# Kernel tuning notes

Measured on AMD Instinct MI355X. Metric: run time of the kernel, lower is better.

Reference implementation:

```python
import jax, jax.numpy as jnp
import numpy as np
import math

NO, NR, E = 100000, 1000, 1000000
DO, DR, DE, H, OM = 64, 32, 4, 64, 32


def setup_inputs() -> dict:
    key = jax.random.key(0)
    ks = jax.random.split(key, 20)
    s = lambda k, sh: jax.random.normal(k, sh, dtype=jnp.float32) * 0.05
    inp = {
        'x_order': jax.random.normal(ks[0], (NO, DO), dtype=jnp.float32),
        'x_rider': jax.random.normal(ks[1], (NR, DR), dtype=jnp.float32),
        'edge_attr': jax.random.normal(ks[2], (E, DE), dtype=jnp.float32),
        'order_idx': jax.random.randint(ks[3], (E,), 0, NO),
        'rider_idx': jax.random.randint(ks[4], (E,), 0, NR),
        'omega_encoded': jax.random.normal(ks[5], (OM,), dtype=jnp.float32),
        # TransformerConv params (heads=1)
        'Wk': s(ks[6], (DO, H)), 'bk': jnp.zeros((H,), jnp.float32),
        'Wq': s(ks[7], (DR, H)), 'bq': jnp.zeros((H,), jnp.float32),
        'Wv': s(ks[8], (DO, H)), 'bv': jnp.zeros((H,), jnp.float32),
        'We': s(ks[9], (DE, H)),  # lin_edge, bias=False in PyG
        'Wskip': s(ks[10], (DR, H)), 'bskip': jnp.zeros((H,), jnp.float32),
        # order_proj
        'Wp': s(ks[11], (DO, H)), 'bp': jnp.zeros((H,), jnp.float32),
        # residual MLP: Linear(2H+OM,128) -> ReLU -> Linear(128,1)
        'W1': s(ks[12], (2 * H + OM, 128)), 'b1': jnp.zeros((128,), jnp.float32),
        'W2': s(ks[13], (128, 1)), 'b2': jnp.zeros((1,), jnp.float32),
    }
    return inp


def _segment_softmax(alpha, seg, num_segments):
    m = jax.ops.segment_max(alpha, seg, num_segments=num_segments)
    m = jnp.where(jnp.isfinite(m), m, 0.0)
    ex = jnp.exp(alpha - m[seg])
    denom = jax.ops.segment_sum(ex, seg, num_segments=num_segments)
    return ex / (denom[seg] + 1e-16)


def reference(x_order, x_rider, edge_attr, order_idx, rider_idx, omega_encoded,
              Wk, bk, Wq, bq, Wv, bv, We, Wskip, bskip, Wp, bp, W1, b1, W2, b2):
    scale = 1.0 / math.sqrt(H)
    # TransformerConv((order, rider) -> rider), heads=1, edge_dim
    q = x_rider @ Wq + bq            # [NR, H]
    k = x_order @ Wk + bk            # [NO, H]
    v = x_order @ Wv + bv            # [NO, H]
    e = edge_attr @ We               # [E, H]
    k_j = k[order_idx] + e           # [E, H]
    v_j = v[order_idx] + e           # [E, H]
    alpha = jnp.sum(q[rider_idx] * k_j, axis=-1) * scale  # [E]
    alpha = _segment_softmax(alpha, rider_idx, NR)
    agg = jax.ops.segment_sum(alpha[:, None] * v_j, rider_idx, num_segments=NR)  # [NR, H]
    rider_emb = agg + x_rider @ Wskip + bskip  # root/skip connection

    # edge scoring
    order_proj = x_order @ Wp + bp   # [NO, H]
    oe = order_proj[order_idx]       # [E, H]
    re = rider_emb[rider_idx]        # [E, H]
    dot = jnp.sum(oe * re, axis=-1) * scale  # [E]
    omega_expand = jnp.broadcast_to(omega_encoded[None, :], (oe.shape[0], OM))
    resid_in = jnp.concatenate([oe, re, omega_expand], axis=-1)  # [E, 2H+OM]
    hmid = jax.nn.relu(resid_in @ W1 + b1)
    resid = (hmid @ W2 + b2)[:, 0]
    return jnp.clip(dot + resid, -10.0, 10.0)
```

## Files before the change

### kernel.cpp

```cpp
#include <hip/hip_runtime.h>
#include <hip/hip_bf16.h>
#include <math.h>
#include <stdint.h>

#define NO_N 100000
#define NR_N 1000
#define E_N  1000000
#define SB     500
#define SCHUNK 2000
#define KVP_TILES 1563
#define KVP_BLKS 1024
#define MAXTILES 17008

typedef short bf16x8 __attribute__((ext_vector_type(8)));
typedef float floatx4 __attribute__((ext_vector_type(4)));

__device__ __forceinline__ unsigned short bfu(float x) {
    union { __hip_bfloat16 h; unsigned short u; } c;
    c.h = __float2bfloat16(x);
    return c.u;
}
__device__ __forceinline__ float bflo(unsigned int u) {
    return __uint_as_float(u << 16);
}
__device__ __forceinline__ float bfhi(unsigned int u) {
    return __uint_as_float(u & 0xffff0000u);
}

__global__ __launch_bounds__(256) void k_front(
    const float* __restrict__ xr,
    const float* __restrict__ Wq, const float* __restrict__ bq,
    const float* __restrict__ Wskip, const float* __restrict__ bskip,
    const float* __restrict__ We,
    float* __restrict__ q, float* __restrict__ skip, float* __restrict__ t,
    const float* __restrict__ W1, const float* __restrict__ b1,
    const float* __restrict__ omega, float* __restrict__ b1eff,
    unsigned short* __restrict__ w1t,
    const float* __restrict__ x,
    const float* __restrict__ Wk, const float* __restrict__ bk,
    const float* __restrict__ Wv, const float* __restrict__ bv,
    const float* __restrict__ Wp, const float* __restrict__ bp,
    unsigned short* __restrict__ kb, unsigned short* __restrict__ vb,
    unsigned short* __restrict__ pb,
    const int* __restrict__ ridx, int* __restrict__ ghist)
{
    __shared__ __align__(16) char smem[9216];
    const int tid = threadIdx.x;
    const int b = blockIdx.x;

    if (b < 250) {
        float* sx = (float*)smem;
        float* sq = sx + 128;
        int rbase = b * 4;
        if (tid < 128) {
            int rl = tid >> 5, d = tid & 31;
            sx[rl * 32 + d] = xr[(rbase + rl) * 32 + d];
        }
        __syncthreads();
        int rl = tid >> 6, h = tid & 63;
        int r = rbase + rl;
        float aq = bq[h], as = bskip[h];
        #pragma unroll 4
        for (int d = 0; d < 32; ++d) {
            float xv = sx[rl * 32 + d];
            aq += xv * Wq[d * 64 + h];
            as += xv * Wskip[d * 64 + h];
        }
        sq[rl * 64 + h] = aq;
        q[r * 64 + h] = aq;
        skip[r * 64 + h] = as;
        __syncthreads();
        if (tid < 16) {
            int rl2 = tid >> 2, d = tid & 3;
            float acc = 0.f;
            for (int hh = 0; hh < 64; ++hh)
                acc += We[d * 64 + hh] * sq[rl2 * 64 + hh];
            t[(rbase + rl2) * 4 + d] = acc;
        }
    } else if (b == 250) {
        if (tid < 128) {
            float acc = b1[tid];
            #pragma unroll 4
            for (int j = 0; j < 32; ++j)
                acc += omega[j] * W1[(128 + j) * 128 + tid];
            b1eff[tid] = acc;
        }
        for (int idx = tid; idx < 64 * 128; idx += 256) {
            int n = idx >> 6, k = idx & 63;
            w1t[idx] = bfu(W1[k * 128 + n]);
        }
    } else if (b < 251 + KVP_BLKS) {
        unsigned short* sX = (unsigned short*)smem;
        const int wave = tid >> 6, lane = tid & 63;
        const int l15 = lane & 15, quad = lane >> 4;

        bf16x8 bfr[3][2];
        float bias[3];
        unsigned short* outT[3];
        int colc[3];
        #pragma unroll
        for (int ct = 0; ct < 3; ++ct) {
            int n = wave * 48 + ct * 16 + l15;
            int table = n >> 6, c = n & 63;
            const float* W  = (table == 0) ? Wk : (table == 1) ? Wv : Wp;
            const float* bb = (table == 0) ? bk : (table == 1) ? bv : bp;
            bias[ct] = bb[c];
            colc[ct] = c;
            outT[ct] = (table == 0) ? kb : (table == 1) ? vb : pb;
            #pragma unroll
            for (int kf = 0; kf < 2; ++kf) {
                bf16x8 f;
                #pragma unroll
                for (int j = 0; j < 8; ++j)
                    f[j] = (short)bfu(W[(size_t)(kf * 32 + quad * 8 + j) * 64 + c]);
                bfr[ct][kf] = f;
            }
        }

        const int srl = tid >> 2;
        const int sqt = (tid & 3) * 16;

        for (int tile = b - 251; tile < KVP_TILES; tile += KVP_BLKS) {
            int rowbase = tile * 64;
            {
                int row = rowbase + srl;
                unsigned short* dst = sX + srl * 72 + sqt;
                if (row < NO_N) {
                    const float4* src = (const float4*)(x + (size_t)row * 64 + sqt);
                    #pragma unroll
                    for (int i = 0; i < 4; ++i) {
                        float4 a = src[i];
                        ushort4 u = { bfu(a.x), bfu(a.y), bfu(a.z), bfu(a.w) };
                        *(ushort4*)(dst + i * 4) = u;
                    }
                } else {
                    ushort4 z = {0, 0, 0, 0};
                    #pragma unroll
                    for (int i = 0; i < 4; ++i) *(ushort4*)(dst + i * 4) = z;
                }
            }
            __syncthreads();

            floatx4 acc[4][3];
            #pragma unroll
            for (int rt = 0; rt < 4; ++rt)
                #pragma unroll
                for (int ct = 0; ct < 3; ++ct)
                    acc[rt][ct] = (floatx4){bias[ct], bias[ct], bias[ct], bias[ct]};

            #pragma unroll
            for (int rt = 0; rt < 4; ++rt) {
                const unsigned short* ar = sX + (size_t)(rt * 16 + l15) * 72 + quad * 8;
                bf16x8 a0 = *(const bf16x8*)(ar);
                bf16x8 a1 = *(const bf16x8*)(ar + 32);
                #pragma unroll
                for (int ct = 0; ct < 3; ++ct) {
                    floatx4 c = acc[rt][ct];
                    c = __builtin_amdgcn_mfma_f32_16x16x32_bf16(a0, bfr[ct][0], c, 0, 0, 0);
                    c = __builtin_amdgcn_mfma_f32_16x16x32_bf16(a1, bfr[ct][1], c, 0, 0, 0);
                    acc[rt][ct] = c;
                }
            }

            #pragma unroll
            for (int rt = 0; rt < 4; ++rt) {
                int rb = rowbase + rt * 16 + quad * 4;
                #pragma unroll
                for (int ct = 0; ct < 3; ++ct) {
                    unsigned short* o = outT[ct];
                    size_t cbase = colc[ct];
                    #pragma unroll
                    for (int g = 0; g < 4; ++g) {
                        int row = rb + g;
                        if (row < NO_N)
                            o[(size_t)row * 64 + cbase] = bfu(acc[rt][ct][g]);
                    }
                }
            }
            __syncthreads();
        }
    } else {
        int* hc = (int*)smem;
        int hb = b - (251 + KVP_BLKS);
        for (int i = tid; i < NR_N; i += 256) hc[i] = 0;
        __syncthreads();
        int s = hb * SCHUNK;
        for (int i = s + tid; i < s + SCHUNK; i += 256)
            atomicAdd(&hc[ridx[i]], 1);
        __syncthreads();
        for (int i = tid; i < NR_N; i += 256)
            ghist[i * SB + hb] = hc[i];
    }
}

__global__ __launch_bounds__(512) void k_colscan(const int* __restrict__ ghist,
                                                 int* __restrict__ gpre,
                                                 int* __restrict__ counts)
{
    __shared__ int s[512];
    int tid = threadIdx.x, r = blockIdx.x;
    int v = (tid < SB) ? ghist[r * SB + tid] : 0;
    s[tid] = v;
    __syncthreads();
    for (int off = 1; off < 512; off <<= 1) {
        int tv = (tid >= off) ? s[tid - off] : 0;
        __syncthreads();
        s[tid] += tv;
        __syncthreads();
    }
    if (tid < SB) gpre[r * SB + tid] = s[tid] - v;
    if (tid == 511) counts[r] = s[511];
}

__global__ __launch_bounds__(1024) void k_scan(const int* __restrict__ counts,
                                               int* __restrict__ offsets,
                                               int* __restrict__ tilestart)
{
    __shared__ int s[1024];
    int tid = threadIdx.x;
    int c = (tid < NR_N) ? counts[tid] : 0;
    s[tid] = c;
    __syncthreads();
    for (int off = 1; off < 1024; off <<= 1) {
        int tv = (tid >= off) ? s[tid - off] : 0;
        __syncthreads();
        s[tid] += tv;
        __syncthreads();
    }
    if (tid < NR_N) offsets[tid] = s[tid] - c;
    if (tid == NR_N - 1) offsets[NR_N] = s[tid];
    __syncthreads();
    int tc = (tid < NR_N) ? ((c + 63) >> 6) : 0;
    s[tid] = tc;
    __syncthreads();
    for (int off = 1; off < 1024; off <<= 1) {
        int tv = (tid >= off) ? s[tid - off] : 0;
        __syncthreads();
        s[tid] += tv;
        __syncthreads();
    }
    if (tid < NR_N) tilestart[tid] = s[tid] - tc;
    if (tid == NR_N - 1) tilestart[NR_N] = s[tid];
}

__global__ __launch_bounds__(256) void k_trec(const int* __restrict__ tilestart,
                                              const int* __restrict__ offsets,
                                              int4* __restrict__ trec)
{
    int nt = tilestart[NR_N];
    int t = blockIdx.x * 256 + threadIdx.x;
    if (t >= nt) return;
    int lo = 0, hi = NR_N - 1;
    while (lo < hi) {
        int mid = (lo + hi + 1) >> 1;
        if (tilestart[mid] <= t) lo = mid; else hi = mid - 1;
    }
    trec[t] = make_int4(lo, offsets[lo] + ((t - tilestart[lo]) << 6),
                        offsets[lo + 1], 0);
}

__global__ __launch_bounds__(1024) void k_scatter2(
    const int* __restrict__ ridx, const int* __restrict__ oidx,
    const float* __restrict__ ea, const float* __restrict__ t,
    const int* __restrict__ offsets, const int* __restrict__ gpre,
    const int* __restrict__ ghist,
    int4* __restrict__ spack, int* __restrict__ so, int* __restrict__ rank)
{
    __shared__ int stmp[1024];
    __shared__ int lpre[NR_N];
    __shared__ int lcur[NR_N];
    __shared__ int gbase[NR_N];
    __shared__ __align__(16) int4 sbuf[SCHUNK];
    __shared__ int spos[SCHUNK];

    const int tid = threadIdx.x, b = blockIdx.x;

    int v = (tid < NR_N) ? ghist[tid * SB + b] : 0;
    stmp[tid] = v;
    __syncthreads();
    for (int off = 1; off < 1024; off <<= 1) {
        int tv = (tid >= off) ? stmp[tid - off] : 0;
        __syncthreads();
        stmp[tid] += tv;
        __syncthreads();
    }
    if (tid < NR_N) {
        lpre[tid] = stmp[tid] - v;
        lcur[tid] = 0;
        gbase[tid] = offsets[tid] + gpre[tid * SB + b];
    }
    __syncthreads();

    int s = b * SCHUNK;
    for (int i = s + tid; i < s + SCHUNK; i += 1024) {
        int r = ridx[i];
        int o = oidx[i];
        float4 e4 = *(const float4*)(ea + (size_t)i * 4);
        float4 t4 = *(const float4*)(t + r * 4);
        float h = e4.x * t4.x + e4.y * t4.y + e4.z * t4.z + e4.w * t4.w;
        int old = atomicAdd(&lcur[r], 1);
        int lpos = lpre[r] + old;
        int gp = gbase[r] + old;
        int4 pk;
        pk.x = o;
        pk.y = __float_as_int(h);
        pk.z = (int)((unsigned)bfu(e4.x) | ((unsigned)bfu(e4.y) << 16));
        pk.w = (int)((unsigned)bfu(e4.z) | ((unsigned)bfu(e4.w) << 16));
        sbuf[lpos] = pk;
        spos[lpos] = gp;
        rank[i] = gp;
    }
    __syncthreads();

    for (int l = tid; l < SCHUNK; l += 1024) {
        int4 pk = sbuf[l];
        int gp = spos[l];
        spack[gp] = pk;
        so[gp] = pk.x;
    }
}

__global__ __launch_bounds__(512) void k_rider(
    const int* __restrict__ offsets, const int4* __restrict__ spack,
    const float* __restrict__ q,
    const unsigned short* __restrict__ kb, const unsigned short* __restrict__ vb,
    const float* __restrict__ We, const float* __restrict__ skip,
    const float* __restrict__ W1, const float* __restrict__ b1eff,
    unsigned short* __restrict__ embb, float* __restrict__ Br)
{
    __shared__ float sQ[64];
    __shared__ int2 sOX[8][64];
    __shared__ float rv[8][64];
    __shared__ float re4[8][4];
    __shared__ float rd[8];

    int r = blockIdx.x;
    int wave = threadIdx.x >> 6, lane = threadIdx.x & 63;
    if (threadIdx.x < 64) sQ[threadIdx.x] = q[r * 64 + threadIdx.x];
    __syncthreads();

    int beg = offsets[r], end = offsets[r + 1];
    int cnt = end - beg;
    int chunk = (cnt + 7) >> 3;
    int s0 = beg + wave * chunk;
    int s1 = min(s0 + chunk, end);

    float av0 = 0.f, av1 = 0.f, av2 = 0.f, av3 = 0.f;
    float dsum = 0.f;
    float ag0 = 0.f, ag1 = 0.f, ag2 = 0.f, ag3 = 0.f;
    const float2* sQ2 = (const float2*)sQ;

    for (int jb = s0; jb < s1; jb += 64) {
        int j = jb + lane;
        bool valid = (j < s1);
        int4 pk = make_int4(0, 0, 0, 0);
        if (valid) pk = spack[j];
        int oo = pk.x;
        float h = __int_as_float(pk.y);

        const uint4* krow = (const uint4*)(kb + (size_t)oo * 64);
        uint4 K0 = krow[0], K1 = krow[1], K2 = krow[2], K3 = krow[3];
        uint4 K4 = krow[4], K5 = krow[5], K6 = krow[6], K7 = krow[7];
        float a0 = h, a1 = 0.f, a2 = 0.f, a3 = 0.f;
        #define DOT8(Kv, base, A) { \
            float2 qa = sQ2[(base) + 0]; \
            A = fmaf(bflo(Kv.x), qa.x, A); A = fmaf(bfhi(Kv.x), qa.y, A); \
            float2 qb = sQ2[(base) + 1]; \
            A = fmaf(bflo(Kv.y), qb.x, A); A = fmaf(bfhi(Kv.y), qb.y, A); \
            float2 qc = sQ2[(base) + 2]; \
            A = fmaf(bflo(Kv.z), qc.x, A); A = fmaf(bfhi(Kv.z), qc.y, A); \
            float2 qd = sQ2[(base) + 3]; \
            A = fmaf(bflo(Kv.w), qd.x, A); A = fmaf(bfhi(Kv.w), qd.y, A); }
        DOT8(K0, 0, a0) DOT8(K1, 4, a1) DOT8(K2, 8, a2) DOT8(K3, 12, a3)
        DOT8(K4, 16, a0) DOT8(K5, 20, a1) DOT8(K6, 24, a2) DOT8(K7, 28, a3)
        #undef DOT8
        float acc = (a0 + a1) + (a2 + a3);

        float exv = valid ? __expf(acc * 0.125f) : 0.f;
        dsum += exv;
        unsigned int ez = (unsigned int)pk.z, ew = (unsigned int)pk.w;
        ag0 = fmaf(exv, bflo(ez), ag0);
        ag1 = fmaf(exv, bfhi(ez), ag1);
        ag2 = fmaf(exv, bflo(ew), ag2);
        ag3 = fmaf(exv, bfhi(ew), ag3);

        sOX[wave][lane] = make_int2(oo, __float_as_int(exv));

        int nn = min(s1 - jb, 64);
        int i = 0;
        for (; i + 8 <= nn; i += 8) {
            int2 x0 = sOX[wave][i + 0], x1 = sOX[wave][i + 1];
            int2 x2 = sOX[wave][i + 2], x3 = sOX[wave][i + 3];
            int2 x4 = sOX[wave][i + 4], x5 = sOX[wave][i + 5];
            int2 x6 = sOX[wave][i + 6], x7 = sOX[wave][i + 7];
            unsigned short u0 = vb[(size_t)x0.x * 64 + lane];
            unsigned short u1 = vb[(size_t)x1.x * 64 + lane];
            unsigned short u2 = vb[(size_t)x2.x * 64 + lane];
            unsigned short u3 = vb[(size_t)x3.x * 64 + lane];
            unsigned short u4 = vb[(size_t)x4.x * 64 + lane];
            unsigned short u5 = vb[(size_t)x5.x * 64 + lane];
            unsigned short u6 = vb[(size_t)x6.x * 64 + lane];
            unsigned short u7 = vb[(size_t)x7.x * 64 + lane];
            av0 = fmaf(__int_as_float(x0.y), __uint_as_float((unsigned int)u0 << 16), av0);
            av1 = fmaf(__int_as_float(x1.y), __uint_as_float((unsigned int)u1 << 16), av1);
            av2 = fmaf(__int_as_float(x2.y), __uint_as_float((unsigned int)u2 << 16), av2);
            av3 = fmaf(__int_as_float(x3.y), __uint_as_float((unsigned int)u3 << 16), av3);
            av0 = fmaf(__int_as_float(x4.y), __uint_as_float((unsigned int)u4 << 16), av0);
            av1 = fmaf(__int_as_float(x5.y), __uint_as_float((unsigned int)u5 << 16), av1);
            av2 = fmaf(__int_as_float(x6.y), __uint_as_float((unsigned int)u6 << 16), av2);
            av3 = fmaf(__int_as_float(x7.y), __uint_as_float((unsigned int)u7 << 16), av3);
        }
        for (; i < nn; ++i) {
            int2 xx = sOX[wave][i];
            unsigned short uu = vb[(size_t)xx.x * 64 + lane];
            av0 = fmaf(__int_as_float(xx.y), __uint_as_float((unsigned int)uu << 16), av0);
        }
    }

    float aggv = (av0 + av1) + (av2 + av3);

    #pragma unroll
    for (int m = 1; m < 64; m <<= 1) {
        dsum += __shfl_xor(dsum, m);
        ag0 += __shfl_xor(ag0, m);
        ag1 += __shfl_xor(ag1, m);
        ag2 += __shfl_xor(ag2, m);
        ag3 += __shfl_xor(ag3, m);
    }

    rv[wave][lane] = aggv;
    if (lane == 0) {
        rd[wave] = dsum;
        re4[wave][0] = ag0; re4[wave][1] = ag1;
        re4[wave][2] = ag2; re4[wave][3] = ag3;
    }
    __syncthreads();
    if (threadIdx.x < 64) {
        int l = threadIdx.x;
        float av = 0.f, ds = 0.f, a0 = 0.f, a1 = 0.f, a2 = 0.f, a3 = 0.f;
        #pragma unroll
        for (int w = 0; w < 8; ++w) {
            av += rv[w][l]; ds += rd[w];
            a0 += re4[w][0]; a1 += re4[w][1]; a2 += re4[w][2]; a3 += re4[w][3];
        }
        float corr = a0 * We[0 * 64 + l] + a1 * We[1 * 64 + l]
                   + a2 * We[2 * 64 + l] + a3 * We[3 * 64 + l];
        float val = (av + corr) / (ds + 1e-16f) + skip[r * 64 + l];
        embb[r * 64 + l] = bfu(val);
        sQ[l] = val;
    }
    __syncthreads();
    if (threadIdx.x < 128) {
        int c = threadIdx.x;
        float a = b1eff[c];
        #pragma unroll 8
        for (int d = 0; d < 64; ++d)
            a = fmaf(sQ[d], W1[(size_t)(64 + d) * 128 + c], a);
        Br[r * 128 + c] = a;
    }
}

__global__ __launch_bounds__(256) void k_edge2(
    const int* __restrict__ so, const int4* __restrict__ trec,
    const int* __restrict__ tilestart,
    const unsigned short* __restrict__ pb, const unsigned short* __restrict__ embb,
    const float* __restrict__ Br, const unsigned short* __restrict__ w1t,
    const float* __restrict__ W2, const float* __restrict__ b2,
    float* __restrict__ tmp)
{
    const int tid = threadIdx.x;
    const int wave = tid >> 6;
    const int lane = tid & 63;
    const int l15 = lane & 15;
    const int quad = lane >> 4;

    bf16x8 bfr[8][2];
    floatx4 w2q[8];
    #pragma unroll
    for (int ctl = 0; ctl < 8; ++ctl) {
        int n = ctl * 16 + l15;
        bfr[ctl][0] = *(const bf16x8*)(w1t + n * 64 + quad * 8);
        bfr[ctl][1] = *(const bf16x8*)(w1t + n * 64 + 32 + quad * 8);
        w2q[ctl] = *(const floatx4*)(W2 + ctl * 16 + quad * 4);
    }
    float b2v = b2[0];
    const int ntiles = tilestart[NR_N];
    const bf16x8 z8 = (bf16x8){0, 0, 0, 0, 0, 0, 0, 0};

    union U4B { uint4 u; bf16x8 b; };

    const int stride = gridDim.x * 4;
    int tile = blockIdx.x * 4 + wave;
    if (tile >= ntiles) return;

    int4 rr = trec[tile];
    int o_rt[4];
    #pragma unroll
    for (int rt = 0; rt < 4; ++rt)
        o_rt[rt] = so[min(rr.y + rt * 16 + l15, rr.z - 1)];

    for (; tile < ntiles; tile += stride) {
        const int r = rr.x, jb = rr.y, jend = rr.z;

        U4B A0[4], A1[4];
        #pragma unroll
        for (int rt = 0; rt < 4; ++rt) {
            const unsigned short* rowp = pb + (size_t)o_rt[rt] * 64 + quad * 8;
            A0[rt].u = *(const uint4*)(rowp);
            A1[rt].u = *(const uint4*)(rowp + 32);
        }

        int4 rrn = trec[min(tile + stride, ntiles - 1)];
        int o_nx[4];
        #pragma unroll
        for (int rt = 0; rt < 4; ++rt)
            o_nx[rt] = so[min(rrn.y + rt * 16 + l15, rrn.z - 1)];

        const unsigned short* eb = embb + r * 64;
        bf16x8 b80 = z8, b81 = z8;
        if (l15 == 0) {
            b80 = *(const bf16x8*)(eb + quad * 8);
            b81 = *(const bf16x8*)(eb + 32 + quad * 8);
        }

        const float* brrow = Br + r * 128;

        #pragma unroll
        for (int rt = 0; rt < 4; ++rt) {
            float s = 0.f;
            #pragma unroll
            for (int ctl = 0; ctl < 8; ++ctl) {
                floatx4 c = *(const floatx4*)(brrow + ctl * 16 + quad * 4);
                c = __builtin_amdgcn_mfma_f32_16x16x32_bf16(bfr[ctl][0], A0[rt].b, c, 0, 0, 0);
                c = __builtin_amdgcn_mfma_f32_16x16x32_bf16(bfr[ctl][1], A1[rt].b, c, 0, 0, 0);
                #pragma unroll
                for (int g = 0; g < 4; ++g)
                    s = fmaf(fmaxf(c[g], 0.f), w2q[ctl][g], s);
            }
            floatx4 c8 = (floatx4){0.f, 0.f, 0.f, 0.f};
            c8 = __builtin_amdgcn_mfma_f32_16x16x32_bf16(b80, A0[rt].b, c8, 0, 0, 0);
            c8 = __builtin_amdgcn_mfma_f32_16x16x32_bf16(b81, A1[rt].b, c8, 0, 0, 0);

            s += __shfl_xor(s, 16);
            s += __shfl_xor(s, 32);

            if (quad == 0) {
                int pos = jb + rt * 16 + l15;
                if (pos < jend) {
                    float v = s + 0.125f * c8[0] + b2v;
                    tmp[pos] = fminf(fmaxf(v, -10.f), 10.f);
                }
            }
        }

        rr = rrn;
        #pragma unroll
        for (int rt = 0; rt < 4; ++rt) o_rt[rt] = o_nx[rt];
    }
}

__global__ __launch_bounds__(256) void k_perm(const int* __restrict__ rank,
                                              const float* __restrict__ tmp,
                                              float* __restrict__ out)
{
    int i = blockIdx.x * 256 + threadIdx.x;
    if (i < E_N) out[i] = tmp[rank[i]];
}

extern "C" void kernel_launch(void* const* d_in, const int* in_sizes, int n_in,
                              void* d_out, int out_size, void* d_ws, size_t ws_size,
                              hipStream_t stream)
{
    const float* x_order   = (const float*)d_in[0];
    const float* x_rider   = (const float*)d_in[1];
    const float* edge_attr = (const float*)d_in[2];
    const int*   order_idx = (const int*)d_in[3];
    const int*   rider_idx = (const int*)d_in[4];
    const float* omega     = (const float*)d_in[5];
    const float* Wk = (const float*)d_in[6];  const float* bk = (const float*)d_in[7];
    const float* Wq = (const float*)d_in[8];  const float* bq = (const float*)d_in[9];
    const float* Wv = (const float*)d_in[10]; const float* bv = (const float*)d_in[11];
    const float* We = (const float*)d_in[12];
    const float* Wskip = (const float*)d_in[13]; const float* bskip = (const float*)d_in[14];
    const float* Wp = (const float*)d_in[15]; const float* bp = (const float*)d_in[16];
    const float* W1 = (const float*)d_in[17]; const float* b1 = (const float*)d_in[18];
    const float* W2 = (const float*)d_in[19]; const float* b2 = (const float*)d_in[20];
    float* out = (float*)d_out;

    unsigned short* ws_kb = (unsigned short*)d_ws;
    unsigned short* ws_vb = ws_kb + (size_t)NO_N * 64;
    unsigned short* ws_pb = ws_vb + (size_t)NO_N * 64;
    int4* ws_spack = (int4*)(ws_pb + (size_t)NO_N * 64);
    float* ws_tmp  = (float*)ws_spack;
    int*  ws_so    = (int*)(ws_spack + E_N);
    int*  ws_rank  = ws_so + E_N;
    float* wsf     = (float*)(ws_rank + E_N);
    float* ws_q    = wsf;
    float* ws_skip = ws_q + NR_N * 64;
    unsigned short* ws_embb = (unsigned short*)(ws_skip + NR_N * 64);
    float* ws_t    = (float*)(ws_embb + NR_N * 64);
    float* ws_b1e  = ws_t + NR_N * 4;
    unsigned short* ws_w1t = (unsigned short*)(ws_b1e + 128);
    float* ws_Br   = (float*)(ws_w1t + 128 * 64);
    int* ws_counts  = (int*)(ws_Br + NR_N * 128);
    int* ws_offsets = ws_counts + NR_N;
    int* ws_tilest  = ws_offsets + NR_N + 8;
    int* ws_ghist   = ws_tilest + NR_N + 8;
    int* ws_gpre    = ws_ghist + NR_N * SB;
    int4* ws_trec   = (int4*)(((uintptr_t)(ws_gpre + NR_N * SB) + 15) & ~(uintptr_t)15);

    k_front<<<251 + KVP_BLKS + SB, 256, 0, stream>>>(
        x_rider, Wq, bq, Wskip, bskip, We, ws_q, ws_skip, ws_t,
        W1, b1, omega, ws_b1e, ws_w1t,
        x_order, Wk, bk, Wv, bv, Wp, bp, ws_kb, ws_vb, ws_pb,
        rider_idx, ws_ghist);
    k_colscan<<<NR_N, 512, 0, stream>>>(ws_ghist, ws_gpre, ws_counts);
    k_scan<<<1, 1024, 0, stream>>>(ws_counts, ws_offsets, ws_tilest);
    k_trec<<<(MAXTILES + 255) / 256, 256, 0, stream>>>(ws_tilest, ws_offsets, ws_trec);
    k_scatter2<<<SB, 1024, 0, stream>>>(rider_idx, order_idx, edge_attr, ws_t,
                                        ws_offsets, ws_gpre, ws_ghist,
                                        ws_spack, ws_so, ws_rank);
    k_rider<<<NR_N, 512, 0, stream>>>(ws_offsets, ws_spack, ws_q,
                                      ws_kb, ws_vb, We, ws_skip,
                                      W1, ws_b1e, ws_embb, ws_Br);
    k_edge2<<<1024, 256, 0, stream>>>(ws_so, ws_trec, ws_tilest,
                                      ws_pb, ws_embb, ws_Br, ws_w1t, W2, b2, ws_tmp);
    k_perm<<<(E_N + 255) / 256, 256, 0, stream>>>(ws_rank, ws_tmp, out);
}
```

Measured before the change: 276.4 us.

## Fuse column scan with global scan via last-block pattern, merge trec into scatter

Result: slower. 508.4 us (+83.9%).

```diff
diff --git a/kernel.cpp b/kernel.cpp
--- a/kernel.cpp
+++ b/kernel.cpp
@@ -6,11 +6,12 @@
 #define NO_N 100000
 #define NR_N 1000
 #define E_N  1000000
-#define SB     500
-#define SCHUNK 2000
+#define SB     250
+#define SCHUNK 4000
 #define KVP_TILES 1563
 #define KVP_BLKS 1024
 #define MAXTILES 17008
+#define TREC_BLKS ((MAXTILES + 1023) / 1024)
 
 typedef short bf16x8 __attribute__((ext_vector_type(8)));
 typedef float floatx4 __attribute__((ext_vector_type(4)));
@@ -42,7 +43,8 @@
     const float* __restrict__ Wp, const float* __restrict__ bp,
     unsigned short* __restrict__ kb, unsigned short* __restrict__ vb,
     unsigned short* __restrict__ pb,
-    const int* __restrict__ ridx, int* __restrict__ ghist)
+    const int* __restrict__ ridx, int* __restrict__ ghist,
+    int* __restrict__ done)
 {
     __shared__ __align__(16) char smem[9216];
     const int tid = threadIdx.x;
@@ -78,6 +80,7 @@
             t[(rbase + rl2) * 4 + d] = acc;
         }
     } else if (b == 250) {
+        if (tid == 0) done[0] = 0;
         if (tid < 128) {
             float acc = b1[tid];
             #pragma unroll 4
@@ -193,31 +196,36 @@
     }
 }
 
-__global__ __launch_bounds__(512) void k_colscan(const int* __restrict__ ghist,
-                                                 int* __restrict__ gpre,
-                                                 int* __restrict__ counts)
+__global__ __launch_bounds__(1024) void k_mid(
+    const int* __restrict__ ghist, int* __restrict__ gpre,
+    int* __restrict__ counts, int* __restrict__ offsets,
+    int* __restrict__ tilestart, int* __restrict__ done)
 {
-    __shared__ int s[512];
-    int tid = threadIdx.x, r = blockIdx.x;
+    __shared__ int s[1024];
+    __shared__ int lastFlag;
+    const int tid = threadIdx.x, r = blockIdx.x;
+
     int v = (tid < SB) ? ghist[r * SB + tid] : 0;
     s[tid] = v;
     __syncthreads();
-    for (int off = 1; off < 512; off <<= 1) {
+    for (int off = 1; off < 1024; off <<= 1) {
         int tv = (tid >= off) ? s[tid - off] : 0;
         __syncthreads();
         s[tid] += tv;
         __syncthreads();
     }
     if (tid < SB) gpre[r * SB + tid] = s[tid] - v;
-    if (tid == 511) counts[r] = s[511];
-}
-
-__global__ __launch_bounds__(1024) void k_scan(const int* __restrict__ counts,
-                                               int* __restrict__ offsets,
-                                               int* __restrict__ tilestart)
-{
-    __shared__ int s[1024];
-    int tid = threadIdx.x;
+    if (tid == 1023) counts[r] = s[1023];
+
+    __threadfence();
+    if (tid == 0) {
+        int old = atomicAdd(done, 1);
+        lastFlag = (old == NR_N - 1);
+    }
+    __syncthreads();
+    if (!lastFlag) return;
+    __threadfence();
+
     int c = (tid < NR_N) ? counts[tid] : 0;
     s[tid] = c;
     __syncthreads();
@@ -241,22 +249,6 @@
     }
     if (tid < NR_N) tilestart[tid] = s[tid] - tc;
     if (tid == NR_N - 1) tilestart[NR_N] = s[tid];
-}
-
-__global__ __launch_bounds__(256) void k_trec(const int* __restrict__ tilestart,
-                                              const int* __restrict__ offsets,
-                                              int4* __restrict__ trec)
-{
-    int nt = tilestart[NR_N];
-    int t = blockIdx.x * 256 + threadIdx.x;
-    if (t >= nt) return;
-    int lo = 0, hi = NR_N - 1;
-    while (lo < hi) {
-        int mid = (lo + hi + 1) >> 1;
-        if (tilestart[mid] <= t) lo = mid; else hi = mid - 1;
-    }
-    trec[t] = make_int4(lo, offsets[lo] + ((t - tilestart[lo]) << 6),
-                        offsets[lo + 1], 0);
 }
 
 __global__ __launch_bounds__(1024) void k_scatter2(
@@ -264,16 +256,31 @@
     const float* __restrict__ ea, const float* __restrict__ t,
     const int* __restrict__ offsets, const int* __restrict__ gpre,
     const int* __restrict__ ghist,
-    int4* __restrict__ spack, int* __restrict__ so, int* __restrict__ rank)
+    int4* __restrict__ spack, int* __restrict__ so, int* __restrict__ rank,
+    const int* __restrict__ tilestart, int4* __restrict__ trec)
 {
+    const int tid = threadIdx.x, b = blockIdx.x;
+
+    if (b >= SB) {
+        int nt = tilestart[NR_N];
+        int tt = (b - SB) * 1024 + tid;
+        if (tt >= nt) return;
+        int lo = 0, hi = NR_N - 1;
+        while (lo < hi) {
+            int mid = (lo + hi + 1) >> 1;
+            if (tilestart[mid] <= tt) lo = mid; else hi = mid - 1;
+        }
+        trec[tt] = make_int4(lo, offsets[lo] + ((tt - tilestart[lo]) << 6),
+                             offsets[lo + 1], 0);
+        return;
+    }
+
     __shared__ int stmp[1024];
     __shared__ int lpre[NR_N];
     __shared__ int lcur[NR_N];
     __shared__ int gbase[NR_N];
     __shared__ __align__(16) int4 sbuf[SCHUNK];
     __shared__ int spos[SCHUNK];
-
-    const int tid = threadIdx.x, b = blockIdx.x;
 
     int v = (tid < NR_N) ? ghist[tid * SB + b] : 0;
     stmp[tid] = v;
@@ -607,19 +614,20 @@
     int* ws_tilest  = ws_offsets + NR_N + 8;
     int* ws_ghist   = ws_tilest + NR_N + 8;
     int* ws_gpre    = ws_ghist + NR_N * SB;
-    int4* ws_trec   = (int4*)(((uintptr_t)(ws_gpre + NR_N * SB) + 15) & ~(uintptr_t)15);
+    int* ws_done    = ws_gpre + NR_N * SB;
+    int4* ws_trec   = (int4*)(((uintptr_t)(ws_done + 8) + 15) & ~(uintptr_t)15);
 
     k_front<<<251 + KVP_BLKS + SB, 256, 0, stream>>>(
         x_rider, Wq, bq, Wskip, bskip, We, ws_q, ws_skip, ws_t,
         W1, b1, omega, ws_b1e, ws_w1t,
         x_order, Wk, bk, Wv, bv, Wp, bp, ws_kb, ws_vb, ws_pb,
-        rider_idx, ws_ghist);
-    k_colscan<<<NR_N, 512, 0, stream>>>(ws_ghist, ws_gpre, ws_counts);
-    k_scan<<<1, 1024, 0, stream>>>(ws_counts, ws_offsets, ws_tilest);
-    k_trec<<<(MAXTILES + 255) / 256, 256, 0, stream>>>(ws_tilest, ws_offsets, ws_trec);
-    k_scatter2<<<SB, 1024, 0, stream>>>(rider_idx, order_idx, edge_attr, ws_t,
-                                        ws_offsets, ws_gpre, ws_ghist,
-                                        ws_spack, ws_so, ws_rank);
+        rider_idx, ws_ghist, ws_done);
+    k_mid<<<NR_N, 1024, 0, stream>>>(ws_ghist, ws_gpre, ws_counts,
+                                     ws_offsets, ws_tilest, ws_done);
+    k_scatter2<<<SB + TREC_BLKS, 1024, 0, stream>>>(
+        rider_idx, order_idx, edge_attr, ws_t,
+        ws_offsets, ws_gpre, ws_ghist, ws_spack, ws_so, ws_rank,
+        ws_tilest, ws_trec);
     k_rider<<<NR_N, 512, 0, stream>>>(ws_offsets, ws_spack, ws_q,
                                       ws_kb, ws_vb, We, ws_skip,
                                       W1, ws_b1e, ws_embb, ws_Br);
```
